# Performance work log

Hardware: AMD Instinct MI355X
Metric: run time of the kernel (lower is better)

The kernel has to match this reference:

```python
import jax, jax.numpy as jnp
import numpy as np


def setup_inputs() -> dict:
    key = jax.random.key(0)
    ks = jax.random.split(key, 6)
    B, N, D, E, S, H = 4, 4096, 768, 4, 1024, 3072
    sc = lambda d: 1.0 / np.sqrt(d)
    return {
        "x": jax.random.normal(ks[0], (B, N, D), dtype=jnp.float32),
        "phi": jax.random.normal(ks[1], (E, S, D), dtype=jnp.float32) * sc(D),
        "w1": jax.random.normal(ks[2], (E, D, H), dtype=jnp.float32) * sc(D),
        "b1": jnp.zeros((E, H), dtype=jnp.float32),
        "w2": jax.random.normal(ks[3], (E, H, D), dtype=jnp.float32) * sc(H),
        "b2": jnp.zeros((E, D), dtype=jnp.float32),
    }


def reference(x, phi, w1, b1, w2, b2):
    # x: [B,N,D], phi: [E,S,D]
    logits = jnp.einsum('bnd,esd->bnes', x, phi)          # [B,N,E,S]
    B, N, E, S = logits.shape
    dispatch = jax.nn.softmax(logits, axis=1)             # softmax over tokens
    combine = jax.nn.softmax(
        logits.reshape(B, N, E * S), axis=-1
    ).reshape(B, N, E, S)                                 # softmax over all slots
    slots = jnp.einsum('bnd,bnes->besd', x, dispatch)     # [B,E,S,D]
    h = jax.nn.gelu(jnp.einsum('besd,edh->besh', slots, w1) + b1[None, :, None, :])
    y = jnp.einsum('besh,ehd->besd', h, w2) + b2[None, :, None, :]
    out = jnp.einsum('besd,bnes->bnd', y, combine)        # [B,N,D]
    return out
```

## Files before the change

kernel.cpp:

```cpp
#include <hip/hip_runtime.h>
#include <hip/hip_bf16.h>

using u16 = unsigned short;
using short8 = __attribute__((ext_vector_type(8))) short;
using floatx4 = __attribute__((ext_vector_type(4))) float;

#define DEVI static __device__ __forceinline__

constexpr int cB = 4, cN = 4096, cD = 768, cE = 4, cS = 1024, cH = 3072;
constexpr int cES = cE * cS;
constexpr int cHC = cH / 2;

DEVI u16 f2bf(float f) {
  union { float f; unsigned u; } v; v.f = f;
  unsigned r = v.u + 0x7fffu + ((v.u >> 16) & 1u);
  return (u16)(r >> 16);
}
DEVI float bf2f(u16 b) {
  union { unsigned u; float f; } v; v.u = ((unsigned)b) << 16;
  return v.f;
}
DEVI float gelu_tanh(float x) {
  float z = 1.5957691216057308f * (x + 0.044715f * x * x * x);
  z = fminf(fmaxf(z, -30.f), 30.f);
  float e = __expf(z);
  float t = (e - 1.f) / (e + 1.f);
  return 0.5f * x * (1.f + t);
}

DEVI void glds16(const u16* g, u16* l) {
  __builtin_amdgcn_global_load_lds(
      (const __attribute__((address_space(1))) void*)g,
      (__attribute__((address_space(3))) void*)l, 16, 0, 0);
}

__global__ __launch_bounds__(256) void zero_kernel(float* __restrict__ p, int n) {
  int i = blockIdx.x * 256 + threadIdx.x;
  if (i < n) p[i] = 0.f;
}

__global__ __launch_bounds__(256) void convert_kernel(const float* __restrict__ in,
                                                      u16* __restrict__ out, long n) {
  long stride = (long)gridDim.x * 256 * 4;
  for (long idx = ((long)blockIdx.x * 256 + threadIdx.x) * 4; idx < n; idx += stride) {
    float4 v = *(const float4*)(in + idx);
    ushort4 o;
    o.x = f2bf(v.x); o.y = f2bf(v.y); o.z = f2bf(v.z); o.w = f2bf(v.w);
    *(ushort4*)(out + idx) = o;
  }
}

DEVI u16 to_bf(float f) { return f2bf(f); }
DEVI u16 to_bf(u16 u) { return u; }

template <typename Tin>
__global__ __launch_bounds__(256) void transpose_bf16_kernel(const Tin* __restrict__ in,
                                                             u16* __restrict__ out,
                                                             int R, int C,
                                                             long strideIn, long strideOut) {
  __shared__ u16 tile[64][65];
  const Tin* inb = in + (long)blockIdx.z * strideIn;
  u16* outb = out + (long)blockIdx.z * strideOut;
  const int r0 = blockIdx.y * 64, c0 = blockIdx.x * 64;
  const int tid = threadIdx.x;
#pragma unroll
  for (int i = 0; i < 16; i++) {
    int idx = i * 256 + tid;
    int r = idx >> 6, c = idx & 63;
    tile[r][c] = to_bf(inb[(long)(r0 + r) * C + (c0 + c)]);
  }
  __syncthreads();
#pragma unroll
  for (int i = 0; i < 16; i++) {
    int idx = i * 256 + tid;
    int r = idx >> 6, c = idx & 63;
    outb[(long)(c0 + r) * R + (r0 + c)] = tile[c][r];
  }
}

template <int EPI>
__global__ __launch_bounds__(256, 2) void gemm_nt(const u16* __restrict__ A,
                                                  const u16* __restrict__ Bm,
                                                  void* __restrict__ Cout,
                                                  int M, int Nn, int K,
                                                  long ldA, long ldB, long ldC,
                                                  long strideA, long strideB, int modB,
                                                  long strideC,
                                                  const float* __restrict__ epiVec,
                                                  long epiStride, int epiMod) {
  __shared__ u16 lds[4 * 8192];

  const int gx = gridDim.x;
  const int nwg = gx * gridDim.y;
  int flat = blockIdx.y * gx + blockIdx.x;
  if ((nwg & 7) == 0) flat = (flat & 7) * (nwg >> 3) + (flat >> 3);
  const int bxs = flat % gx, bys = flat / gx;

  const int bz = blockIdx.z;
  const u16* Ab = A + (long)bz * strideA;
  const u16* Bb = Bm + (long)(bz % modB) * strideB;
  const float* ev = epiVec + (long)(bz % epiMod) * epiStride;
  const int tileM = bys * 128, tileN = bxs * 128;
  const int tid = threadIdx.x;
  const int wave = tid >> 6, lane = tid & 63;
  const int quad = lane >> 4, l16 = lane & 15;
  const int wm = (wave >> 1) * 64, wn = (wave & 1) * 64;

  const int swzk = (((lane & 3) ^ ((lane >> 3) & 3)) << 3);
  const int r0 = wave * 32 + (lane >> 2);
  const u16* aG0 = Ab + (long)(tileM + r0) * ldA + swzk;
  const u16* aG1 = Ab + (long)(tileM + r0 + 16) * ldA + swzk;
  const u16* bG0 = Bb + (long)(tileN + r0) * ldB + swzk;
  const u16* bG1 = Bb + (long)(tileN + r0 + 16) * ldB + swzk;
  const int ldsW = wave * 1024;

  const int NT = K >> 5;

  auto STAGE = [&](int tt) {
    u16* l = &lds[(tt & 3) * 8192];
    const long ko = (long)tt << 5;
    glds16(aG0 + ko, l + ldsW);
    glds16(aG1 + ko, l + ldsW + 512);
    glds16(bG0 + ko, l + 4096 + ldsW);
    glds16(bG1 + ko, l + 4096 + ldsW + 512);
  };

  floatx4 acc[4][4] = {};
  const int sread = ((quad ^ ((l16 >> 1) & 3)) << 3);

  STAGE(0);
  if (NT > 1) STAGE(1);
  if (NT > 2) STAGE(2);

  for (int t = 0; t < NT; t++) {
    asm volatile("s_barrier" ::: "memory");
    if (t + 3 < NT) STAGE(t + 3);
    const int ahead = NT - 1 - t;
    if (ahead >= 3)      asm volatile("s_waitcnt vmcnt(12)" ::: "memory");
    else if (ahead == 2) asm volatile("s_waitcnt vmcnt(8)" ::: "memory");
    else if (ahead == 1) asm volatile("s_waitcnt vmcnt(4)" ::: "memory");
    else                 asm volatile("s_waitcnt vmcnt(0)" ::: "memory");
    asm volatile("s_barrier" ::: "memory");

    const u16* As = &lds[(t & 3) * 8192];
    const u16* Bs = As + 4096;
    short8 af[4], bq[4];
#pragma unroll
    for (int i = 0; i < 4; i++)
      af[i] = *(const short8*)&As[(wm + i * 16 + l16) * 32 + sread];
#pragma unroll
    for (int j = 0; j < 4; j++)
      bq[j] = *(const short8*)&Bs[(wn + j * 16 + l16) * 32 + sread];
    __builtin_amdgcn_s_setprio(1);
#pragma unroll
    for (int i = 0; i < 4; i++)
#pragma unroll
      for (int j = 0; j < 4; j++)
        acc[i][j] = __builtin_amdgcn_mfma_f32_16x16x32_bf16(af[i], bq[j], acc[i][j], 0, 0, 0);
    __builtin_amdgcn_s_setprio(0);
  }

  const long cBase = (long)bz * strideC;
#pragma unroll
  for (int i = 0; i < 4; i++) {
#pragma unroll
    for (int r = 0; r < 4; r++) {
      const int row = tileM + wm + i * 16 + quad * 4 + r;
      float rscale = 1.f;
      if (EPI == 1 || EPI == 4) rscale = 1.f / ev[row];
#pragma unroll
      for (int j = 0; j < 4; j++) {
        const int col = tileN + wn + j * 16 + l16;
        float v = acc[i][j][r];
        const long cIdx = cBase + (long)row * ldC + col;
        if (EPI == 0) v = __expf(v);
        if (EPI == 1 || EPI == 4) v *= rscale;
        if (EPI == 2) v = gelu_tanh(v + ev[col]);
        if (EPI == 3) v = v + ev[col];
        if (EPI == 5) v = v + bf2f(((u16*)Cout)[cIdx]);
        if (EPI == 4)
          ((float*)Cout)[cIdx] = v;
        else
          ((u16*)Cout)[cIdx] = f2bf(v);
      }
    }
  }
}

template <int EPI>
__global__ __launch_bounds__(512, 2) void gemm256(const u16* __restrict__ A,
                                                  const u16* __restrict__ Bm,
                                                  void* __restrict__ Cout,
                                                  int M, int Nn, int K,
                                                  long ldA, long ldB, long ldC,
                                                  long strideA, long strideB, int modB,
                                                  long strideC,
                                                  const float* __restrict__ epiVec,
                                                  long epiStride, int epiMod,
                                                  float* __restrict__ Zc,
                                                  float* __restrict__ Zr) {
  __shared__ u16 lds[2][2][2][8192];

  const int gx = gridDim.x;
  const int nwg = gx * gridDim.y;
  int flat = blockIdx.y * gx + blockIdx.x;
  {
    const int q = nwg >> 3, r = nwg & 7, xc = flat & 7, o = flat >> 3;
    flat = (xc < r ? xc * (q + 1) : r * (q + 1) + (xc - r) * q) + o;
  }
  const int bxs = flat % gx, bys = flat / gx;

  const int bz = blockIdx.z;
  const u16* __restrict__ Ab = A + (long)bz * strideA;
  const u16* __restrict__ Bb = Bm + (long)(bz % modB) * strideB;
  const float* __restrict__ ev = epiVec + (long)(bz % epiMod) * epiStride;
  const int tileM = bys * 256, tileN = bxs * 256;
  const int tid = threadIdx.x;
  const int wave = tid >> 6, lane = tid & 63;
  const int quad = lane >> 4, l16 = lane & 15;
  const int wr = wave >> 2, wc = wave & 3;

  const int kswz = (((lane & 3) ^ ((lane >> 3) & 3)) << 3);
  const int srow = wave * 32 + (lane >> 2);
  const u16* gA = Ab + (long)(tileM + srow) * ldA + kswz;
  const u16* gB = Bb + (long)(tileN + srow) * ldB + kswz;

  const int rdsw = ((quad ^ ((l16 >> 1) & 3)) << 3);
  const int aOff = (wr * 128 + l16) * 32 + rdsw;
  const int bOff = (wc * 64 + l16) * 32 + rdsw;

  const int NT = K >> 6;

#define STA256(buf, kh, tt) do {                                   \
    const u16* _g = gA + ((long)(tt) << 6) + ((kh) << 5);          \
    u16* _l = &lds[buf][0][kh][wave * 1024];                       \
    glds16(_g, _l); glds16(_g + 16 * ldA, _l + 512); } while (0)
#define STB256(buf, kh, tt) do {                                   \
    const u16* _g = gB + ((long)(tt) << 6) + ((kh) << 5);          \
    u16* _l = &lds[buf][1][kh][wave * 1024];                       \
    glds16(_g, _l); glds16(_g + 16 * ldB, _l + 512); } while (0)
#define BAR256 asm volatile("s_barrier" ::: "memory")
#define LGK0   asm volatile("s_waitcnt lgkmcnt(0)" ::: "memory")

  floatx4 acc[8][4] = {};
  short8 af[4], bq[4];

  STA256(0, 0, 0); STB256(0, 0, 0); STA256(0, 1, 0); STB256(0, 1, 0);
  STB256(1, 0, 1); STA256(1, 0, 1); STB256(1, 1, 1);
  asm volatile("s_waitcnt vmcnt(6)" ::: "memory");
  BAR256;

#define TILE256(kt, buf) do {                                                      \
    const bool s1 = (kt) + 1 < NT, s2 = (kt) + 2 < NT;                             \
                                            \
    _Pragma("unroll") for (int i = 0; i < 4; i++)                                  \
      af[i] = *(const short8*)&lds[buf][0][0][aOff + i * 512];                     \
    _Pragma("unroll") for (int n = 0; n < 4; n++)                                  \
      bq[n] = *(const short8*)&lds[buf][1][0][bOff + n * 512];                     \
    if (s1) STA256((buf) ^ 1, 1, (kt) + 1);                                        \
    BAR256; LGK0;                                                                  \
    __builtin_amdgcn_s_setprio(1);                                                 \
    _Pragma("unroll") for (int i = 0; i < 4; i++)                                  \
      _Pragma("unroll") for (int n = 0; n < 4; n++)                                \
        acc[i][n] = __builtin_amdgcn_mfma_f32_16x16x32_bf16(af[i], bq[n], acc[i][n], 0, 0, 0); \
    __builtin_amdgcn_s_setprio(0);                                                 \
    BAR256;                                                                        \
                                         \
    _Pragma("unroll") for (int i = 0; i < 4; i++)                                  \
      af[i] = *(const short8*)&lds[buf][0][0][aOff + (4 + i) * 512];               \
    if (s2) STB256(buf, 0, (kt) + 2);                                              \
    BAR256; LGK0;                                                                  \
    __builtin_amdgcn_s_setprio(1);                                                 \
    _Pragma("unroll") for (int i = 0; i < 4; i++)                                  \
      _Pragma("unroll") for (int n = 0; n < 4; n++)                                \
        acc[4 + i][n] = __builtin_amdgcn_mfma_f32_16x16x32_bf16(af[i], bq[n], acc[4 + i][n], 0, 0, 0); \
    __builtin_amdgcn_s_setprio(0);                                                 \
    BAR256;                                                                        \
                                            \
    _Pragma("unroll") for (int i = 0; i < 4; i++)                                  \
      af[i] = *(const short8*)&lds[buf][0][1][aOff + i * 512];                     \
    _Pragma("unroll") for (int n = 0; n < 4; n++)                                  \
      bq[n] = *(const short8*)&lds[buf][1][1][bOff + n * 512];                     \
    if (s2) STA256(buf, 0, (kt) + 2);                                              \
    BAR256; LGK0;                                                                  \
    __builtin_amdgcn_s_setprio(1);                                                 \
    _Pragma("unroll") for (int i = 0; i < 4; i++)                                  \
      _Pragma("unroll") for (int n = 0; n < 4; n++)                                \
        acc[i][n] = __builtin_amdgcn_mfma_f32_16x16x32_bf16(af[i], bq[n], acc[i][n], 0, 0, 0); \
    __builtin_amdgcn_s_setprio(0);                                                 \
    BAR256;                                                                        \
                                                    \
    _Pragma("unroll") for (int i = 0; i < 4; i++)                                  \
      af[i] = *(const short8*)&lds[buf][0][1][aOff + (4 + i) * 512];               \
    if (s2) STB256(buf, 1, (kt) + 2);                                              \
    BAR256; LGK0;                                                                  \
    __builtin_amdgcn_s_setprio(1);                                                 \
    _Pragma("unroll") for (int i = 0; i < 4; i++)                                  \
      _Pragma("unroll") for (int n = 0; n < 4; n++)                                \
        acc[4 + i][n] = __builtin_amdgcn_mfma_f32_16x16x32_bf16(af[i], bq[n], acc[4 + i][n], 0, 0, 0); \
    __builtin_amdgcn_s_setprio(0);                                                 \
    if (s2)      asm volatile("s_waitcnt vmcnt(6)" ::: "memory");                  \
    else if (s1) asm volatile("s_waitcnt vmcnt(0)" ::: "memory");                  \
    BAR256;                                                                        \
  } while (0)

  for (int kt = 0; kt < NT; kt += 2) {
    TILE256(kt, 0);
    TILE256(kt + 1, 1);
  }
#undef TILE256
#undef STA256
#undef STB256
#undef BAR256
#undef LGK0

  const long cBase = (long)bz * strideC;
  if (EPI == 6) {
    float csum[4] = {0.f, 0.f, 0.f, 0.f};
#pragma unroll
    for (int m = 0; m < 8; m++) {
#pragma unroll
      for (int r = 0; r < 4; r++) {
        const int row = tileM + wr * 128 + m * 16 + quad * 4 + r;
        float rs = 0.f;
#pragma unroll
        for (int n = 0; n < 4; n++) {
          const int col = tileN + wc * 64 + n * 16 + l16;
          float v = __expf(acc[m][n][r]);
          ((u16*)Cout)[cBase + (long)row * ldC + col] = f2bf(v);
          rs += v;
          csum[n] += v;
        }
        rs += __shfl_xor(rs, 1, 64);
        rs += __shfl_xor(rs, 2, 64);
        rs += __shfl_xor(rs, 4, 64);
        rs += __shfl_xor(rs, 8, 64);
        if (l16 == 0) atomicAdd(&Zr[row], rs);
      }
    }
#pragma unroll
    for (int n = 0; n < 4; n++) {
      float c = csum[n];
      c += __shfl_xor(c, 16, 64);
      c += __shfl_xor(c, 32, 64);
      if (quad == 0) atomicAdd(&Zc[tileN + wc * 64 + n * 16 + l16], c);
    }
  } else {
#pragma unroll
    for (int m = 0; m < 8; m++) {
#pragma unroll
      for (int r = 0; r < 4; r++) {
        const int row = tileM + wr * 128 + m * 16 + quad * 4 + r;
        float rscale = 1.f;
        if (EPI == 1 || EPI == 4) rscale = 1.f / ev[row];
#pragma unroll
        for (int n = 0; n < 4; n++) {
          const int col = tileN + wc * 64 + n * 16 + l16;
          float v = acc[m][n][r];
          const long cIdx = cBase + (long)row * ldC + col;
          if (EPI == 0) v = __expf(v);
          if (EPI == 1 || EPI == 4) v *= rscale;
          if (EPI == 2) v = gelu_tanh(v + ev[col]);
          if (EPI == 3) v = v + ev[col];
          if (EPI == 5) v = v + bf2f(((u16*)Cout)[cIdx]);
          if (EPI == 4)
            ((float*)Cout)[cIdx] = v;
          else
            ((u16*)Cout)[cIdx] = f2bf(v);
        }
      }
    }
  }
}

extern "C" void kernel_launch(void* const* d_in, const int* in_sizes, int n_in,
                              void* d_out, int out_size, void* d_ws, size_t ws_size,
                              hipStream_t stream) {
  const float* x   = (const float*)d_in[0];
  const float* phi = (const float*)d_in[1];
  const float* w1  = (const float*)d_in[2];
  const float* b1  = (const float*)d_in[3];
  const float* w2  = (const float*)d_in[4];
  const float* b2  = (const float*)d_in[5];
  (void)in_sizes; (void)n_in; (void)out_size;
  float* out_f = (float*)d_out;

  char* ws = (char*)d_ws;
  size_t off = 0;
  auto carve = [&](size_t bytes) -> char* {
    char* p = ws + off;
    off += (bytes + 255) & ~(size_t)255;
    return p;
  };

  const size_t SZ_P  = (size_t)cN * cES * 2;
  const size_t SZ_HC = (size_t)cB * cE * cS * cHC * 2;

  const bool cacheP = ws_size >= (size_t)306 * 1024 * 1024;

  u16 *Pall = nullptr, *PtA = nullptr, *HcA = nullptr;
  u16 *Pb = nullptr, *Ptb = nullptr, *HcB = nullptr, *P2 = nullptr;
  if (cacheP) {
    Pall = (u16*)carve(4 * SZ_P);
    char* RPH = carve(SZ_HC);
    PtA = (u16*)RPH; HcA = (u16*)RPH;
  } else {
    char* R1 = carve(2 * SZ_P);
    Pb = (u16*)R1; Ptb = (u16*)(R1 + SZ_P); HcB = (u16*)R1; P2 = (u16*)R1;
  }
  u16* Xbf = (u16*)carve((size_t)cB * cN * cD * 2);
  char* R3r = carve((size_t)cB * cD * cN * 2);
  u16* Xt = (u16*)R3r;
  u16* Yv = (u16*)R3r;
  char* R4r = carve((size_t)cB * cES * cD * 2);
  u16* Slots = (u16*)R4r;
  u16* Yt    = (u16*)R4r;
  u16* Phibf = (u16*)carve((size_t)cES * cD * 2);
  u16* W1t = (u16*)carve((size_t)cE * cH * cD * 2);
  u16* W2t = (u16*)carve((size_t)cE * cD * cH * 2);
  float* Z1 = (float*)carve((size_t)(cB * cES + cB * cN) * 4);
  float* Z2 = Z1 + (size_t)cB * cES;

  convert_kernel<<<2048, 256, 0, stream>>>(x, Xbf, (long)cB * cN * cD);
  convert_kernel<<<1024, 256, 0, stream>>>(phi, Phibf, (long)cES * cD);
  transpose_bf16_kernel<float><<<dim3(cH / 64, cD / 64, cE), 256, 0, stream>>>(
      w1, W1t, cD, cH, (long)cD * cH, (long)cH * cD);
  transpose_bf16_kernel<float><<<dim3(cD / 64, cH / 64, cE), 256, 0, stream>>>(
      w2, W2t, cH, cD, (long)cH * cD, (long)cD * cH);
  transpose_bf16_kernel<float><<<dim3(cD / 64, cN / 64, cB), 256, 0, stream>>>(
      x, Xt, cN, cD, (long)cN * cD, (long)cD * cN);
  zero_kernel<<<(cB * (cES + cN)) / 256, 256, 0, stream>>>(Z1, cB * (cES + cN));

  for (int b = 0; b < cB; b++) {
    const u16* Xb = Xbf + (long)b * cN * cD;
    u16* Pdst = cacheP ? Pall + (size_t)b * cN * cES : Pb;
    u16* Ptmp = cacheP ? PtA : Ptb;
    gemm256<6><<<dim3(cES / 256, cN / 256, 1), 512, 0, stream>>>(
        Xb, Phibf, Pdst, cN, cES, cD, cD, cD, cES,
        0L, 0L, 1, 0L, Z1, 0, 1,
        Z1 + (long)b * cES, Z2 + (long)b * cN);
    transpose_bf16_kernel<u16><<<dim3(cES / 64, cN / 64, 1), 256, 0, stream>>>(
        Pdst, Ptmp, cN, cES, 0L, 0L);
    gemm_nt<1><<<dim3(cD / 128, cES / 128, 1), 256, 0, stream>>>(
        Ptmp, Xt + (long)b * cD * cN, Slots + (long)b * cES * cD,
        cES, cD, cN, cN, cN, cD,
        0L, 0L, 1, 0L, Z1 + (long)b * cES, 0, 1);
  }

  u16* Hc = cacheP ? HcA : HcB;
  for (int hc = 0; hc < 2; hc++) {
    const int h0 = hc * cHC;
    gemm256<2><<<dim3(cHC / 256, cS / 256, cB * cE), 512, 0, stream>>>(
        Slots, W1t + (long)h0 * cD, Hc, cS, cHC, cD, cD, cD, cHC,
        (long)cS * cD, (long)cH * cD, cE, (long)cS * cHC, b1 + h0, cH, cE,
        nullptr, nullptr);
    if (hc == 0)
      gemm256<3><<<dim3(cD / 256, cS / 256, cB * cE), 512, 0, stream>>>(
          Hc, W2t + h0, Yv, cS, cD, cHC, cHC, cH, cD,
          (long)cS * cHC, (long)cD * cH, cE, (long)cS * cD, b2, cD, cE,
          nullptr, nullptr);
    else
      gemm256<5><<<dim3(cD / 256, cS / 256, cB * cE), 512, 0, stream>>>(
          Hc, W2t + h0, Yv, cS, cD, cHC, cHC, cH, cD,
          (long)cS * cHC, (long)cD * cH, cE, (long)cS * cD, b2, cD, cE,
          nullptr, nullptr);
  }

  transpose_bf16_kernel<u16><<<dim3(cD / 64, cES / 64, cB), 256, 0, stream>>>(
      Yv, Yt, cES, cD, (long)cES * cD, (long)cD * cES);
  for (int bp = 0; bp < 2; bp++) {
    const u16* Psrc;
    if (cacheP) {
      Psrc = Pall + (size_t)(bp * 2) * cN * cES;
    } else {
      const u16* Xb = Xbf + (long)(bp * 2) * cN * cD;
      gemm256<0><<<dim3(cES / 256, cN / 256, 2), 512, 0, stream>>>(
          Xb, Phibf, P2, cN, cES, cD, cD, cD, cES,
          (long)cN * cD, 0L, 1, (long)cN * cES, Z1, 0, 1, nullptr, nullptr);
      Psrc = P2;
    }
    gemm_nt<4><<<dim3(cD / 128, cN / 128, 2), 256, 0, stream>>>(
        Psrc, Yt + (long)(bp * 2) * cD * cES, out_f + (long)(bp * 2) * cN * cD,
        cN, cD, cES, cES, cES, cD,
        (long)cN * cES, (long)cD * cES, 2, (long)cN * cD,
        Z2 + (long)(bp * 2) * cN, cN, 2);
  }
}
```

Baseline: 1.096 ms.

## Double-buffer LDS fragment registers to overlap reads with MFMA in GEMM mainloop

Restructures the 256-tile GEMM main loop so fragment loads for the next MFMA group go into a second register set (X/Y ping-pong) while the current group computes. Partial lgkmcnt waits replace full waits, and one barrier per sub-step is removed, so LDS reads can overlap with MFMA issue. The cost is more VGPRs for the extra fragment registers, which may lower occupancy. The wait counts and the barrier placement also become more fragile: LDS buffer reuse now relies on the exact counter values being right.

```diff
diff --git a/kernel.cpp b/kernel.cpp
--- a/kernel.cpp
+++ b/kernel.cpp
@@ -240,68 +240,66 @@
     u16* _l = &lds[buf][1][kh][wave * 1024];                       \
     glds16(_g, _l); glds16(_g + 16 * ldB, _l + 512); } while (0)
 #define BAR256 asm volatile("s_barrier" ::: "memory")
-#define LGK0   asm volatile("s_waitcnt lgkmcnt(0)" ::: "memory")
+#define LGKM(n) asm volatile("s_waitcnt lgkmcnt(" #n ")" ::: "memory")
 
   floatx4 acc[8][4] = {};
-  short8 af[4], bq[4];
+  short8 afX[4], afY[4], bqX[4], bqY[4];
+
+#define MFMA16(afS, bqS, mb)                                                        \
+    __builtin_amdgcn_s_setprio(1);                                                  \
+    _Pragma("unroll") for (int i = 0; i < 4; i++)                                    \
+      _Pragma("unroll") for (int n = 0; n < 4; n++)                                  \
+        acc[(mb) + i][n] =                                                           \
+            __builtin_amdgcn_mfma_f32_16x16x32_bf16(afS[i], bqS[n], acc[(mb)+i][n], 0, 0, 0); \
+    __builtin_amdgcn_s_setprio(0)
 
   STA256(0, 0, 0); STB256(0, 0, 0); STA256(0, 1, 0); STB256(0, 1, 0);
   STB256(1, 0, 1); STA256(1, 0, 1); STB256(1, 1, 1);
   asm volatile("s_waitcnt vmcnt(6)" ::: "memory");
   BAR256;
-
-#define TILE256(kt, buf) do {                                                      \
-    const bool s1 = (kt) + 1 < NT, s2 = (kt) + 2 < NT;                             \
-                                            \
-    _Pragma("unroll") for (int i = 0; i < 4; i++)                                  \
-      af[i] = *(const short8*)&lds[buf][0][0][aOff + i * 512];                     \
-    _Pragma("unroll") for (int n = 0; n < 4; n++)                                  \
-      bq[n] = *(const short8*)&lds[buf][1][0][bOff + n * 512];                     \
-    if (s1) STA256((buf) ^ 1, 1, (kt) + 1);                                        \
-    BAR256; LGK0;                                                                  \
-    __builtin_amdgcn_s_setprio(1);                                                 \
-    _Pragma("unroll") for (int i = 0; i < 4; i++)                                  \
-      _Pragma("unroll") for (int n = 0; n < 4; n++)                                \
-        acc[i][n] = __builtin_amdgcn_mfma_f32_16x16x32_bf16(af[i], bq[n], acc[i][n], 0, 0, 0); \
-    __builtin_amdgcn_s_setprio(0);                                                 \
-    BAR256;                                                                        \
-                                         \
-    _Pragma("unroll") for (int i = 0; i < 4; i++)                                  \
-      af[i] = *(const short8*)&lds[buf][0][0][aOff + (4 + i) * 512];               \
-    if (s2) STB256(buf, 0, (kt) + 2);                                              \
-    BAR256; LGK0;                                                                  \
-    __builtin_amdgcn_s_setprio(1);                                                 \
-    _Pragma("unroll") for (int i = 0; i < 4; i++)                                  \
-      _Pragma("unroll") for (int n = 0; n < 4; n++)                                \
-        acc[4 + i][n] = __builtin_amdgcn_mfma_f32_16x16x32_bf16(af[i], bq[n], acc[4 + i][n], 0, 0, 0); \
-    __builtin_amdgcn_s_setprio(0);                                                 \
-    BAR256;                                                                        \
-                                            \
-    _Pragma("unroll") for (int i = 0; i < 4; i++)                                  \
-      af[i] = *(const short8*)&lds[buf][0][1][aOff + i * 512];                     \
-    _Pragma("unroll") for (int n = 0; n < 4; n++)                                  \
-      bq[n] = *(const short8*)&lds[buf][1][1][bOff + n * 512];                     \
-    if (s2) STA256(buf, 0, (kt) + 2);                                              \
-    BAR256; LGK0;                                                                  \
-    __builtin_amdgcn_s_setprio(1);                                                 \
-    _Pragma("unroll") for (int i = 0; i < 4; i++)                                  \
-      _Pragma("unroll") for (int n = 0; n < 4; n++)                                \
-        acc[i][n] = __builtin_amdgcn_mfma_f32_16x16x32_bf16(af[i], bq[n], acc[i][n], 0, 0, 0); \
-    __builtin_amdgcn_s_setprio(0);                                                 \
-    BAR256;                                                                        \
-                                                    \
-    _Pragma("unroll") for (int i = 0; i < 4; i++)                                  \
-      af[i] = *(const short8*)&lds[buf][0][1][aOff + (4 + i) * 512];               \
-    if (s2) STB256(buf, 1, (kt) + 2);                                              \
-    BAR256; LGK0;                                                                  \
-    __builtin_amdgcn_s_setprio(1);                                                 \
-    _Pragma("unroll") for (int i = 0; i < 4; i++)                                  \
-      _Pragma("unroll") for (int n = 0; n < 4; n++)                                \
-        acc[4 + i][n] = __builtin_amdgcn_mfma_f32_16x16x32_bf16(af[i], bq[n], acc[4 + i][n], 0, 0, 0); \
-    __builtin_amdgcn_s_setprio(0);                                                 \
-    if (s2)      asm volatile("s_waitcnt vmcnt(6)" ::: "memory");                  \
-    else if (s1) asm volatile("s_waitcnt vmcnt(0)" ::: "memory");                  \
-    BAR256;                                                                        \
+#pragma unroll
+  for (int i = 0; i < 4; i++) afX[i] = *(const short8*)&lds[0][0][0][aOff + i * 512];
+#pragma unroll
+  for (int n = 0; n < 4; n++) bqX[n] = *(const short8*)&lds[0][1][0][bOff + n * 512];
+
+#define TILE256(kt, buf) do {                                                        \
+    const bool s1 = (kt) + 1 < NT, s2 = (kt) + 2 < NT;                               \
+                                                                            \
+    _Pragma("unroll") for (int i = 0; i < 4; i++)                                    \
+      afY[i] = *(const short8*)&lds[buf][0][0][aOff + (4 + i) * 512];                \
+    if (s1) STA256((buf) ^ 1, 1, (kt) + 1);                                          \
+    LGKM(4);                                                                         \
+    MFMA16(afX, bqX, 0);                                                             \
+    BAR256;                                                                          \
+                                                                            \
+    _Pragma("unroll") for (int i = 0; i < 4; i++)                                    \
+      afX[i] = *(const short8*)&lds[buf][0][1][aOff + i * 512];                      \
+    _Pragma("unroll") for (int n = 0; n < 4; n++)                                    \
+      bqY[n] = *(const short8*)&lds[buf][1][1][bOff + n * 512];                      \
+    if (s2) STB256(buf, 0, (kt) + 2);                                                \
+    LGKM(8);                                                                         \
+    MFMA16(afY, bqX, 4);                                                             \
+    BAR256;                                                                          \
+                                                                            \
+    _Pragma("unroll") for (int i = 0; i < 4; i++)                                    \
+      afY[i] = *(const short8*)&lds[buf][0][1][aOff + (4 + i) * 512];                \
+    if (s2) STA256(buf, 0, (kt) + 2);                                                \
+    LGKM(4);                                                                         \
+    MFMA16(afX, bqY, 0);                                                             \
+    if (s2) asm volatile("s_waitcnt vmcnt(4)" ::: "memory");                         \
+    else    asm volatile("s_waitcnt vmcnt(0)" ::: "memory");                         \
+    BAR256;                                                                          \
+                                                                            \
+    if (s1) {                                                                        \
+      _Pragma("unroll") for (int i = 0; i < 4; i++)                                  \
+        afX[i] = *(const short8*)&lds[(buf) ^ 1][0][0][aOff + i * 512];              \
+      _Pragma("unroll") for (int n = 0; n < 4; n++)                                  \
+        bqX[n] = *(const short8*)&lds[(buf) ^ 1][1][0][bOff + n * 512];              \
+    }                                                                                \
+    if (s2) STB256(buf, 1, (kt) + 2);                                                \
+    if (s1) { LGKM(8); } else { LGKM(0); }                                           \
+    MFMA16(afY, bqY, 4);                                                             \
+    BAR256;                                                                          \
   } while (0)
 
   for (int kt = 0; kt < NT; kt += 2) {
@@ -309,10 +307,11 @@
     TILE256(kt + 1, 1);
   }
 #undef TILE256
+#undef MFMA16
 #undef STA256
 #undef STB256
 #undef BAR256
-#undef LGK0
+#undef LGKM
 
   const long cBase = (long)bz * strideC;
   if (EPI == 6) {
```

New measurement: 1.429 ms. +30.3%, slower.

## Alias workspace buffers to enable P caching at smaller sizes; vectorize transpose

Applied to the files above, without the earlier changes.

Reworks the workspace layout so the cached-P path needs less memory: Xbf shares storage with W2t and Phibf with W1t. The weight transposes move to after the dispatch stage, once those buffers are dead. The FFN is split into 2 or 4 hidden chunks depending on available workspace. The transpose kernel now uses float4/ushort4 vector loads and stores with a padded LDS tile, to cut memory transactions. The intent is to enable P caching, which avoids recomputing the logits GEMM, when the workspace is below the old 306MB threshold. The risk is that the extra chunks raise kernel-launch and GEMM tail overhead.

```diff
diff --git a/kernel.cpp b/kernel.cpp
--- a/kernel.cpp
+++ b/kernel.cpp
@@ -9,7 +9,6 @@
 
 constexpr int cB = 4, cN = 4096, cD = 768, cE = 4, cS = 1024, cH = 3072;
 constexpr int cES = cE * cS;
-constexpr int cHC = cH / 2;
 
 DEVI u16 f2bf(float f) {
   union { float f; unsigned u; } v; v.f = f;
@@ -50,31 +49,39 @@
   }
 }
 
-DEVI u16 to_bf(float f) { return f2bf(f); }
-DEVI u16 to_bf(u16 u) { return u; }
-
 template <typename Tin>
 __global__ __launch_bounds__(256) void transpose_bf16_kernel(const Tin* __restrict__ in,
                                                              u16* __restrict__ out,
                                                              int R, int C,
                                                              long strideIn, long strideOut) {
-  __shared__ u16 tile[64][65];
+  __shared__ u16 tile[64][66];
   const Tin* inb = in + (long)blockIdx.z * strideIn;
   u16* outb = out + (long)blockIdx.z * strideOut;
   const int r0 = blockIdx.y * 64, c0 = blockIdx.x * 64;
   const int tid = threadIdx.x;
 #pragma unroll
-  for (int i = 0; i < 16; i++) {
-    int idx = i * 256 + tid;
-    int r = idx >> 6, c = idx & 63;
-    tile[r][c] = to_bf(inb[(long)(r0 + r) * C + (c0 + c)]);
+  for (int i = 0; i < 4; i++) {
+    int v = i * 256 + tid;
+    int r = v >> 4, c4 = (v & 15) * 4;
+    if constexpr (sizeof(Tin) == 4) {
+      float4 f = *(const float4*)&inb[(long)(r0 + r) * C + (c0 + c4)];
+      tile[r][c4 + 0] = f2bf(f.x); tile[r][c4 + 1] = f2bf(f.y);
+      tile[r][c4 + 2] = f2bf(f.z); tile[r][c4 + 3] = f2bf(f.w);
+    } else {
+      ushort4 u = *(const ushort4*)&inb[(long)(r0 + r) * C + (c0 + c4)];
+      tile[r][c4 + 0] = u.x; tile[r][c4 + 1] = u.y;
+      tile[r][c4 + 2] = u.z; tile[r][c4 + 3] = u.w;
+    }
   }
   __syncthreads();
 #pragma unroll
-  for (int i = 0; i < 16; i++) {
-    int idx = i * 256 + tid;
-    int r = idx >> 6, c = idx & 63;
-    outb[(long)(c0 + r) * R + (r0 + c)] = tile[c][r];
+  for (int i = 0; i < 4; i++) {
+    int w = i * 256 + tid;
+    int orow = w >> 4, oc4 = (w & 15) * 4;
+    ushort4 u;
+    u.x = tile[oc4 + 0][orow]; u.y = tile[oc4 + 1][orow];
+    u.z = tile[oc4 + 2][orow]; u.w = tile[oc4 + 3][orow];
+    *(ushort4*)&outb[(long)(c0 + orow) * R + (r0 + oc4)] = u;
   }
 }
 
@@ -393,42 +400,57 @@
     return p;
   };
 
-  const size_t SZ_P  = (size_t)cN * cES * 2;
-  const size_t SZ_HC = (size_t)cB * cE * cS * cHC * 2;
-
-  const bool cacheP = ws_size >= (size_t)306 * 1024 * 1024;
-
-  u16 *Pall = nullptr, *PtA = nullptr, *HcA = nullptr;
-  u16 *Pb = nullptr, *Ptb = nullptr, *HcB = nullptr, *P2 = nullptr;
+  const size_t SZ_P = (size_t)cN * cES * 2;
+
+  int nChunk = 2;
+  bool cacheP = false;
+  if (ws_size >= (size_t)279200000)      { cacheP = true; nChunk = 2; }
+  else if (ws_size >= (size_t)262400000) { cacheP = true; nChunk = 4; }
+  const int cHCx = cH / nChunk;
+
+  u16 *Pall = nullptr, *PtA = nullptr;
+  u16 *Pb = nullptr, *Ptb = nullptr, *P2 = nullptr;
+  u16 *Hc, *Xbf, *Xt, *Yv, *Slots, *Yt, *Phibf, *W1t, *W2t;
+  float *Z1, *Z2;
+
   if (cacheP) {
     Pall = (u16*)carve(4 * SZ_P);
-    char* RPH = carve(SZ_HC);
-    PtA = (u16*)RPH; HcA = (u16*)RPH;
+    const size_t hcBytes = (size_t)cB * cE * cS * cHCx * 2;
+    char* RS = carve(SZ_P > hcBytes ? SZ_P : hcBytes);
+    PtA = (u16*)RS; Hc = (u16*)RS;
+    char* XW2 = carve((size_t)cB * cN * cD * 2);
+    Xbf = (u16*)XW2; W2t = (u16*)XW2;
+    char* R3r = carve((size_t)cB * cD * cN * 2);
+    Xt = (u16*)R3r; Yv = (u16*)R3r;
+    char* R4r = carve((size_t)cB * cES * cD * 2);
+    Slots = (u16*)R4r; Yt = (u16*)R4r;
+    char* PW1 = carve((size_t)cE * cH * cD * 2);
+    Phibf = (u16*)PW1; W1t = (u16*)PW1;
   } else {
     char* R1 = carve(2 * SZ_P);
-    Pb = (u16*)R1; Ptb = (u16*)(R1 + SZ_P); HcB = (u16*)R1; P2 = (u16*)R1;
-  }
-  u16* Xbf = (u16*)carve((size_t)cB * cN * cD * 2);
-  char* R3r = carve((size_t)cB * cD * cN * 2);
-  u16* Xt = (u16*)R3r;
-  u16* Yv = (u16*)R3r;
-  char* R4r = carve((size_t)cB * cES * cD * 2);
-  u16* Slots = (u16*)R4r;
-  u16* Yt    = (u16*)R4r;
-  u16* Phibf = (u16*)carve((size_t)cES * cD * 2);
-  u16* W1t = (u16*)carve((size_t)cE * cH * cD * 2);
-  u16* W2t = (u16*)carve((size_t)cE * cD * cH * 2);
-  float* Z1 = (float*)carve((size_t)(cB * cES + cB * cN) * 4);
-  float* Z2 = Z1 + (size_t)cB * cES;
+    Pb = (u16*)R1; Ptb = (u16*)(R1 + SZ_P); Hc = (u16*)R1; P2 = (u16*)R1;
+    Xbf = (u16*)carve((size_t)cB * cN * cD * 2);
+    char* R3r = carve((size_t)cB * cD * cN * 2);
+    Xt = (u16*)R3r; Yv = (u16*)R3r;
+    char* R4r = carve((size_t)cB * cES * cD * 2);
+    Slots = (u16*)R4r; Yt = (u16*)R4r;
+    Phibf = (u16*)carve((size_t)cES * cD * 2);
+    W1t = (u16*)carve((size_t)cE * cH * cD * 2);
+    W2t = (u16*)carve((size_t)cE * cD * cH * 2);
+  }
+  Z1 = (float*)carve((size_t)(cB * cES + cB * cN) * 4);
+  Z2 = Z1 + (size_t)cB * cES;
 
   convert_kernel<<<2048, 256, 0, stream>>>(x, Xbf, (long)cB * cN * cD);
   convert_kernel<<<1024, 256, 0, stream>>>(phi, Phibf, (long)cES * cD);
-  transpose_bf16_kernel<float><<<dim3(cH / 64, cD / 64, cE), 256, 0, stream>>>(
-      w1, W1t, cD, cH, (long)cD * cH, (long)cH * cD);
-  transpose_bf16_kernel<float><<<dim3(cD / 64, cH / 64, cE), 256, 0, stream>>>(
-      w2, W2t, cH, cD, (long)cH * cD, (long)cD * cH);
   transpose_bf16_kernel<float><<<dim3(cD / 64, cN / 64, cB), 256, 0, stream>>>(
       x, Xt, cN, cD, (long)cN * cD, (long)cD * cN);
+  if (!cacheP) {
+    transpose_bf16_kernel<float><<<dim3(cH / 64, cD / 64, cE), 256, 0, stream>>>(
+        w1, W1t, cD, cH, (long)cD * cH, (long)cH * cD);
+    transpose_bf16_kernel<float><<<dim3(cD / 64, cH / 64, cE), 256, 0, stream>>>(
+        w2, W2t, cH, cD, (long)cH * cD, (long)cD * cH);
+  }
   zero_kernel<<<(cB * (cES + cN)) / 256, 256, 0, stream>>>(Z1, cB * (cES + cN));
 
   for (int b = 0; b < cB; b++) {
@@ -447,22 +469,28 @@
         0L, 0L, 1, 0L, Z1 + (long)b * cES, 0, 1);
   }
 
-  u16* Hc = cacheP ? HcA : HcB;
-  for (int hc = 0; hc < 2; hc++) {
-    const int h0 = hc * cHC;
-    gemm256<2><<<dim3(cHC / 256, cS / 256, cB * cE), 512, 0, stream>>>(
-        Slots, W1t + (long)h0 * cD, Hc, cS, cHC, cD, cD, cD, cHC,
-        (long)cS * cD, (long)cH * cD, cE, (long)cS * cHC, b1 + h0, cH, cE,
+  if (cacheP) {
+    transpose_bf16_kernel<float><<<dim3(cH / 64, cD / 64, cE), 256, 0, stream>>>(
+        w1, W1t, cD, cH, (long)cD * cH, (long)cH * cD);
+    transpose_bf16_kernel<float><<<dim3(cD / 64, cH / 64, cE), 256, 0, stream>>>(
+        w2, W2t, cH, cD, (long)cH * cD, (long)cD * cH);
+  }
+
+  for (int hc = 0; hc < nChunk; hc++) {
+    const int h0 = hc * cHCx;
+    gemm256<2><<<dim3(cHCx / 256, cS / 256, cB * cE), 512, 0, stream>>>(
+        Slots, W1t + (long)h0 * cD, Hc, cS, cHCx, cD, cD, cD, cHCx,
+        (long)cS * cD, (long)cH * cD, cE, (long)cS * cHCx, b1 + h0, cH, cE,
         nullptr, nullptr);
     if (hc == 0)
       gemm256<3><<<dim3(cD / 256, cS / 256, cB * cE), 512, 0, stream>>>(
-          Hc, W2t + h0, Yv, cS, cD, cHC, cHC, cH, cD,
-          (long)cS * cHC, (long)cD * cH, cE, (long)cS * cD, b2, cD, cE,
+          Hc, W2t + h0, Yv, cS, cD, cHCx, cHCx, cH, cD,
+          (long)cS * cHCx, (long)cD * cH, cE, (long)cS * cD, b2, cD, cE,
           nullptr, nullptr);
     else
       gemm256<5><<<dim3(cD / 256, cS / 256, cB * cE), 512, 0, stream>>>(
-          Hc, W2t + h0, Yv, cS, cD, cHC, cHC, cH, cD,
-          (long)cS * cHC, (long)cD * cH, cE, (long)cS * cD, b2, cD, cE,
+          Hc, W2t + h0, Yv, cS, cD, cHCx, cHCx, cH, cD,
+          (long)cS * cHCx, (long)cD * cH, cE, (long)cS * cD, b2, cD, cE,
           nullptr, nullptr);
   }
 
```

Result: faster. 1.059 ms (-3.4%).
